# Optimization experiments

Measured on AMD Instinct MI355X. Metric: run time of the kernel, lower is better.

The kernel has to match this reference:

```python
import jax, jax.numpy as jnp
import numpy as np

B, S, E, H, C = 32, 256, 768, 512, 30
IN0 = E + 2  # LSTM layer-0 input size (770)


def _lstm_dir(x_sbf, Wih, Whh, bih, bhh, reverse):
    """One LSTM direction. x_sbf: [S,B,F]. PyTorch gate order i,f,g,o. Returns [S,B,H]."""
    h0 = jnp.zeros((x_sbf.shape[1], Whh.shape[1]), x_sbf.dtype)
    c0 = jnp.zeros_like(h0)
    xW = jnp.einsum('sbf,gf->sbg', x_sbf, Wih) + (bih + bhh)  # precompute input proj

    def step(carry, xw_t):
        h, c = carry
        gates = xw_t + h @ Whh.T
        i, f, g, o = jnp.split(gates, 4, axis=-1)
        c = jax.nn.sigmoid(f) * c + jax.nn.sigmoid(i) * jnp.tanh(g)
        h = jax.nn.sigmoid(o) * jnp.tanh(c)
        return (h, c), h

    _, ys = jax.lax.scan(step, (h0, c0), xW, reverse=reverse)
    return ys  # aligned with input time order


def _bilstm_layer(x_sbf, Wf, Uf, bif, bhf, Wb, Ub, bib, bhb):
    hf = _lstm_dir(x_sbf, Wf, Uf, bif, bhf, reverse=False)
    hb = _lstm_dir(x_sbf, Wb, Ub, bib, bhb, reverse=True)
    return jnp.concatenate([hf, hb], axis=-1)  # [S,B,2H]


def setup_inputs() -> dict:
    key = jax.random.key(0)
    ks = jax.random.split(key, 24)
    d = {
        'hidden_states': jax.random.normal(ks[0], (4, B, S, E), jnp.float32),
        'roles': jax.random.randint(ks[1], (B, S), 0, C),
        'predicates': jax.random.randint(ks[2], (B, S), 0, 2),
    }
    G = 4 * H
    shapes = {
        'Wih_l0f': (G, IN0), 'Whh_l0f': (G, H), 'bih_l0f': (G,), 'bhh_l0f': (G,),
        'Wih_l0b': (G, IN0), 'Whh_l0b': (G, H), 'bih_l0b': (G,), 'bhh_l0b': (G,),
        'Wih_l1f': (G, 2 * H), 'Whh_l1f': (G, H), 'bih_l1f': (G,), 'bhh_l1f': (G,),
        'Wih_l1b': (G, 2 * H), 'Whh_l1b': (G, H), 'bih_l1b': (G,), 'bhh_l1b': (G,),
        'W_out': (C, 2 * H), 'b_out': (C,),
    }
    for i, (name, shp) in enumerate(shapes.items()):
        d[name] = jax.random.normal(ks[3 + i], shp, jnp.float32) * 0.05
    return d


def reference(hidden_states, roles, predicates,
              Wih_l0f, Whh_l0f, bih_l0f, bhh_l0f,
              Wih_l0b, Whh_l0b, bih_l0b, bhh_l0b,
              Wih_l1f, Whh_l1f, bih_l1f, bhh_l1f,
              Wih_l1b, Whh_l1b, bih_l1b, bhh_l1b,
              W_out, b_out):
    # mean of last-4 transformer hidden states: [B,S,E]
    out = hidden_states.mean(axis=0)
    # vectorized predicate-relative features (replaces the Python .item() loops)
    idx_pred = jnp.argmax(predicates, axis=-1)                      # [B]
    mean_word = out.mean(axis=-1)                                   # [B,S]
    mean_pred = jnp.take_along_axis(mean_word, idx_pred[:, None], axis=1)  # [B,1]
    delta = mean_word - mean_pred                                   # [B,S]
    role_mask = ((roles != 0) & (roles != -100)).astype(out.dtype)  # [B,S]
    x = jnp.concatenate([out, delta[..., None], role_mask[..., None]], axis=-1)  # [B,S,E+2]

    # 2-layer BiLSTM (eval mode; inter-layer dropout inactive)
    x = jnp.swapaxes(x, 0, 1)  # [S,B,F]
    x = _bilstm_layer(x, Wih_l0f, Whh_l0f, bih_l0f, bhh_l0f,
                      Wih_l0b, Whh_l0b, bih_l0b, bhh_l0b)
    x = _bilstm_layer(x, Wih_l1f, Whh_l1f, bih_l1f, bhh_l1f,
                      Wih_l1b, Whh_l1b, bih_l1b, bhh_l1b)
    x = jnp.swapaxes(x, 0, 1)  # [B,S,2H]
    return x @ W_out.T + b_out  # [B,S,classes]
```

## Files before the change

kernel.cpp:

```cpp
#include <hip/hip_runtime.h>
#include <hip/hip_bf16.h>
#include <math.h>

#define BB 32
#define SS 256
#define EE 768
#define HH 512
#define GG 2048
#define NCLS 30
#define NWG 16

typedef __attribute__((ext_vector_type(8))) short bf16x8;
typedef __attribute__((ext_vector_type(4))) float f32x4;
typedef unsigned long long u64;

__device__ inline unsigned short f2bf(float f) {
  union { float f; unsigned int u; } v; v.f = f;
  unsigned int r = v.u + 0x7fffu + ((v.u >> 16) & 1u);
  return (unsigned short)(r >> 16);
}
__device__ inline float bf2f(unsigned short u) {
  union { unsigned int u; float f; } v; v.u = ((unsigned int)u) << 16;
  return v.f;
}
__device__ inline float sigm(float x) { return 1.f / (1.f + expf(-x)); }

__device__ inline void load_lds16(const void* g, void* l) {
  __builtin_amdgcn_global_load_lds(
      (const __attribute__((address_space(1))) void*)g,
      (__attribute__((address_space(3))) void*)l, 16, 0, 0);
}

__device__ inline u64 aload64(const u64* p) {
  return __hip_atomic_load(p, __ATOMIC_RELAXED, __HIP_MEMORY_SCOPE_AGENT);
}
__device__ inline void astore64(u64* p, u64 v) {
  __hip_atomic_store(p, v, __ATOMIC_RELAXED, __HIP_MEMORY_SCOPE_AGENT);
}

__global__ void k_convpad(const float* __restrict__ src, unsigned short* __restrict__ dst,
                          int R, int Ks, int Kd) {
  int n = R * Kd;
  for (int i = blockIdx.x * blockDim.x + threadIdx.x; i < n; i += gridDim.x * blockDim.x) {
    int r = i / Kd, k = i - r * Kd;
    dst[i] = (k < Ks) ? f2bf(src[(size_t)r * Ks + k]) : (unsigned short)0;
  }
}

__global__ void k_biassum(const float* __restrict__ a, const float* __restrict__ b,
                          float* __restrict__ o) {
  int i = blockIdx.x * 256 + threadIdx.x;
  if (i < GG) o[i] = a[i] + b[i];
}

__global__ void k_hinit(u64* __restrict__ h0, u64* __restrict__ h1) {
  int i = blockIdx.x * 256 + threadIdx.x;
  if (i < 16384) {
    u64 v = ((i >> 12) & 1) ? 0x0001000100010001ULL : 0ULL;
    h0[i] = v;
    h1[i] = v;
  }
}

__global__ void k_idxpred(const int* __restrict__ pred, int* __restrict__ idxp) {
  int b = blockIdx.x, l = threadIdx.x;
  const int* pb = pred + b * SS;
  int4 v = *(const int4*)(pb + l * 4);
  int loc = 0x7fffffff;
  if (v.w == 1) loc = 4 * l + 3;
  if (v.z == 1) loc = 4 * l + 2;
  if (v.y == 1) loc = 4 * l + 1;
  if (v.x == 1) loc = 4 * l + 0;
  for (int off = 32; off > 0; off >>= 1) {
    int o = __shfl_down(loc, off);
    loc = min(loc, o);
  }
  if (l == 0) idxp[b] = (loc == 0x7fffffff) ? 0 : loc;
}

__global__ void k_buildA0(const float* __restrict__ hs, const int* __restrict__ roles,
                          float* __restrict__ mw, unsigned short* __restrict__ A0) {
  int blk = blockIdx.x;
  int s = blk >> 5, b = blk & 31;
  unsigned short* row = A0 + (size_t)blk * 800;
  size_t base = ((size_t)b * SS + s) * EE;
  const size_t LSTR = (size_t)BB * SS * EE;
  __shared__ float red[256];
  float part = 0.f;
  for (int k = threadIdx.x; k < EE; k += 256) {
    float v = (hs[base + k] + hs[base + LSTR + k] + hs[base + 2 * LSTR + k] +
               hs[base + 3 * LSTR + k]) * 0.25f;
    part += v;
    row[k] = f2bf(v);
  }
  red[threadIdx.x] = part;
  __syncthreads();
  for (int s2 = 128; s2 > 0; s2 >>= 1) {
    if (threadIdx.x < s2) red[threadIdx.x] += red[threadIdx.x + s2];
    __syncthreads();
  }
  if (threadIdx.x == 0) mw[b * SS + s] = red[0] * (1.f / 768.f);
  if (threadIdx.x == 1) {
    int rl = roles[b * SS + s];
    row[769] = f2bf((rl != 0 && rl != -100) ? 1.f : 0.f);
  }
  if (threadIdx.x < 30) row[770 + threadIdx.x] = 0;
}

__global__ void k_predfeat(const float* __restrict__ mw, const int* __restrict__ idxp,
                           unsigned short* __restrict__ A0) {
  int i = blockIdx.x * 256 + threadIdx.x;
  int b = i >> 8, s = i & 255;
  float d = mw[i] - mw[b * SS + idxp[b]];
  A0[(size_t)(s * 32 + b) * 800 + 768] = f2bf(d);
}

__global__ __launch_bounds__(256) void k_gemm_bt(const unsigned short* __restrict__ A,
                                                 const unsigned short* __restrict__ W,
                                                 const float* __restrict__ bias,
                                                 float* __restrict__ C, int K) {
  __shared__ unsigned short As[128 * 32];
  __shared__ unsigned short Bs[128 * 32];
  const int tid = threadIdx.x;
  const int wave = tid >> 6, lane = tid & 63;
  const int l15 = lane & 15, quad = lane >> 4;
  const int m0 = blockIdx.y * 128, n0 = blockIdx.x * 128;
  const int wr = (wave >> 1) * 64, wc = (wave & 1) * 64;
  const int srow = wave * 16 + (lane >> 2);
  const int scol = (lane & 3) * 8;

  f32x4 acc[4][4];
#pragma unroll
  for (int i = 0; i < 4; i++)
#pragma unroll
    for (int j = 0; j < 4; j++) acc[i][j] = (f32x4){0.f, 0.f, 0.f, 0.f};

  for (int k0 = 0; k0 < K; k0 += 32) {
#pragma unroll
    for (int rep = 0; rep < 2; rep++) {
      load_lds16(A + (size_t)(m0 + rep * 64 + srow) * K + k0 + scol,
                 &As[(rep * 64 + wave * 16) * 32]);
      load_lds16(W + (size_t)(n0 + rep * 64 + srow) * K + k0 + scol,
                 &Bs[(rep * 64 + wave * 16) * 32]);
    }
    __syncthreads();
    bf16x8 af[4], bfr[4];
#pragma unroll
    for (int i = 0; i < 4; i++) af[i] = *(const bf16x8*)&As[(wr + i * 16 + l15) * 32 + quad * 8];
#pragma unroll
    for (int j = 0; j < 4; j++) bfr[j] = *(const bf16x8*)&Bs[(wc + j * 16 + l15) * 32 + quad * 8];
#pragma unroll
    for (int i = 0; i < 4; i++)
#pragma unroll
      for (int j = 0; j < 4; j++)
        acc[i][j] = __builtin_amdgcn_mfma_f32_16x16x32_bf16(af[i], bfr[j], acc[i][j], 0, 0, 0);
    __syncthreads();
  }

#pragma unroll
  for (int j = 0; j < 4; j++) {
    int n = n0 + wc + j * 16 + l15;
    float bv = bias[n];
#pragma unroll
    for (int i = 0; i < 4; i++) {
      int m = m0 + wr + i * 16 + quad * 4;
      int s = m >> 5, b = m & 31;
      f32x4 v = acc[i][j];
      f32x4 outv = {v[0] + bv, v[1] + bv, v[2] + bv, v[3] + bv};
      *(f32x4*)(C + ((size_t)s * GG + n) * BB + b) = outv;
    }
  }
}

__global__ __launch_bounds__(256, 1) void k_recurrent(const float* __restrict__ xWf,
                                                      const float* __restrict__ xWb,
                                                      const unsigned short* __restrict__ WhhF,
                                                      const unsigned short* __restrict__ WhhB,
                                                      u64* __restrict__ hbuf,
                                                      unsigned short* __restrict__ Hout) {
  const int wg = blockIdx.x, dir = wg >> 4, slice = wg & 15;
  const int tid = threadIdx.x, wave = tid >> 6, lane = tid & 63;
  const int l15 = lane & 15, quad = lane >> 4;
  const int u0 = slice * 32;
  const unsigned short* Whh = dir ? WhhB : WhhF;
  const float* xW = dir ? xWb : xWf;
  u64* hbT = hbuf + (size_t)dir * 8192;

  __shared__ __attribute__((aligned(16))) short hlds[32][528];
  __shared__ float gbuf[4][32][32];

  for (int i = tid; i < 32 * 264; i += 256) ((unsigned int*)hlds)[i] = 0;

  bf16x8 bfrag[2][16];
#pragma unroll
  for (int j = 0; j < 2; j++) {
    const unsigned short* wrow = Whh + (size_t)(wave * HH + u0 + j * 16 + l15) * HH + quad * 8;
#pragma unroll
    for (int kk = 0; kk < 16; kk++) bfrag[j][kk] = *(const bf16x8*)(wrow + kk * 32);
  }

  const int cb = tid >> 3;
  const int cu = (tid & 7) * 4;
  float cst[4] = {0.f, 0.f, 0.f, 0.f};

  const int guc = tid & 127;
  const int bb0 = tid >> 7;
  const bool ownCol = ((guc >> 3) == slice);

  f32x4 xv[2][2];
  {
    const int time0 = dir ? (SS - 1) : 0;
#pragma unroll
    for (int j = 0; j < 2; j++)
#pragma unroll
      for (int i = 0; i < 2; i++)
        xv[i][j] = *(const f32x4*)(xW + ((size_t)time0 * GG + wave * HH + u0 + j * 16 + l15) * BB +
                                   i * 16 + quad * 4);
  }
  __syncthreads();

  for (int t = 0; t < SS; t++) {
    const int time = dir ? (SS - 1 - t) : t;

    f32x4 acc[2][2];
#pragma unroll
    for (int i = 0; i < 2; i++)
#pragma unroll
      for (int j = 0; j < 2; j++) acc[i][j] = xv[i][j];

#pragma unroll
    for (int kk = 0; kk < 16; kk++) {
      bf16x8 a0 = *(const bf16x8*)&hlds[l15][quad * 8 + kk * 32];
      bf16x8 a1 = *(const bf16x8*)&hlds[16 + l15][quad * 8 + kk * 32];
      acc[0][0] = __builtin_amdgcn_mfma_f32_16x16x32_bf16(a0, bfrag[0][kk], acc[0][0], 0, 0, 0);
      acc[0][1] = __builtin_amdgcn_mfma_f32_16x16x32_bf16(a0, bfrag[1][kk], acc[0][1], 0, 0, 0);
      acc[1][0] = __builtin_amdgcn_mfma_f32_16x16x32_bf16(a1, bfrag[0][kk], acc[1][0], 0, 0, 0);
      acc[1][1] = __builtin_amdgcn_mfma_f32_16x16x32_bf16(a1, bfrag[1][kk], acc[1][1], 0, 0, 0);
    }
#pragma unroll
    for (int i = 0; i < 2; i++)
#pragma unroll
      for (int j = 0; j < 2; j++)
#pragma unroll
        for (int r = 0; r < 4; r++)
          gbuf[wave][i * 16 + quad * 4 + r][j * 16 + l15] = acc[i][j][r];
    __syncthreads();

    f32x4 G0 = *(const f32x4*)&gbuf[0][cb][cu];
    f32x4 G1 = *(const f32x4*)&gbuf[1][cb][cu];
    f32x4 G2 = *(const f32x4*)&gbuf[2][cb][cu];
    f32x4 G3 = *(const f32x4*)&gbuf[3][cb][cu];
    const unsigned Tb = ((unsigned)(t + 1) >> 1) & 1u;
    unsigned short hs4[4];
#pragma unroll
    for (int q = 0; q < 4; q++) {
      float gi = sigm(G0[q]), gf = sigm(G1[q]), gg = tanhf(G2[q]), go = sigm(G3[q]);
      cst[q] = gf * cst[q] + gi * gg;
      hs4[q] = (unsigned short)((f2bf(go * tanhf(cst[q])) & 0xFFFEu) | Tb);
    }
    const u64 packed =
        (u64)((unsigned)hs4[0] | ((unsigned)hs4[1] << 16)) |
        ((u64)((unsigned)hs4[2] | ((unsigned)hs4[3] << 16)) << 32);

    const int slw = (t + 1) & 1;
    astore64(hbT + slw * 4096 + (cb * 128 + ((u0 + cu) >> 2)), packed);
    *(u64*)&hlds[cb][u0 + cu] = packed;

    *(uint2*)(Hout + ((size_t)time * BB + cb) * 1024 + dir * HH + u0 + cu) =
        make_uint2((unsigned)packed, (unsigned)(packed >> 32));
    {
      const int tn = (t + 1 < SS) ? (t + 1) : t;
      const int timen = dir ? (SS - 1 - tn) : tn;
#pragma unroll
      for (int j = 0; j < 2; j++)
#pragma unroll
        for (int i = 0; i < 2; i++)
          xv[i][j] = *(const f32x4*)(xW + ((size_t)timen * GG + wave * HH + u0 + j * 16 + l15) * BB +
                                     i * 16 + quad * 4);
    }

    if (t + 1 < SS && !ownCol) {
      const u64 tmask = 0x0001000100010001ULL;
      const u64 tpat = Tb ? tmask : 0ULL;
      const u64* src = hbT + slw * 4096;
      u64 v[16];
#pragma unroll
      for (int i = 0; i < 16; i++) v[i] = aload64(src + (bb0 + 2 * i) * 128 + guc);
      for (;;) {
        unsigned st = 0;
#pragma unroll
        for (int i = 0; i < 16; i++)
          if (((v[i] ^ tpat) & tmask) != 0ULL) st |= 1u << i;
        if (!__any(st)) break;
#pragma unroll
        for (int i = 0; i < 16; i++)
          if (st & (1u << i)) v[i] = aload64(src + (bb0 + 2 * i) * 128 + guc);
      }
#pragma unroll
      for (int i = 0; i < 16; i++) *(u64*)&hlds[bb0 + 2 * i][guc * 4] = v[i];
    }
    __syncthreads();
  }
}

__global__ __launch_bounds__(256) void k_out(const unsigned short* __restrict__ H1,
                                             const float* __restrict__ Wout,
                                             const float* __restrict__ bout,
                                             float* __restrict__ out) {
  __shared__ float rows[8][1024];
  __shared__ float ps[8][32][8];
  const int rb = blockIdx.x * 8;
  const int tid = threadIdx.x;
  for (int idx = tid; idx < 8 * 1024; idx += 256) {
    int r = idx >> 10, k = idx & 1023;
    rows[r][k] = bf2f(H1[(size_t)(rb + r) * 1024 + k]);
  }
  __syncthreads();
  const int c = tid & 31, p = tid >> 5;
  float acc[8] = {0.f, 0.f, 0.f, 0.f, 0.f, 0.f, 0.f, 0.f};
  if (c < NCLS) {
    const float* wr = Wout + (size_t)c * 1024 + p * 128;
    for (int k = 0; k < 128; k++) {
      float w = wr[k];
#pragma unroll
      for (int r = 0; r < 8; r++) acc[r] += rows[r][p * 128 + k] * w;
    }
  }
#pragma unroll
  for (int r = 0; r < 8; r++) ps[p][c][r] = acc[r];
  __syncthreads();
  if (p == 0 && c < NCLS) {
    for (int r = 0; r < 8; r++) {
      float v = bout[c];
#pragma unroll
      for (int q = 0; q < 8; q++) v += ps[q][c][r];
      int row = rb + r, s = row >> 5, b = row & 31;
      out[((size_t)b * SS + s) * NCLS + c] = v;
    }
  }
}

extern "C" void kernel_launch(void* const* d_in, const int* in_sizes, int n_in,
                              void* d_out, int out_size, void* d_ws, size_t ws_size,
                              hipStream_t stream) {
  const float* hs     = (const float*)d_in[0];
  const int*   roles  = (const int*)d_in[1];
  const int*   preds  = (const int*)d_in[2];
  const float* Wih0f  = (const float*)d_in[3];
  const float* Whh0f  = (const float*)d_in[4];
  const float* bih0f  = (const float*)d_in[5];
  const float* bhh0f  = (const float*)d_in[6];
  const float* Wih0b  = (const float*)d_in[7];
  const float* Whh0b  = (const float*)d_in[8];
  const float* bih0b  = (const float*)d_in[9];
  const float* bhh0b  = (const float*)d_in[10];
  const float* Wih1f  = (const float*)d_in[11];
  const float* Whh1f  = (const float*)d_in[12];
  const float* bih1f  = (const float*)d_in[13];
  const float* bhh1f  = (const float*)d_in[14];
  const float* Wih1b  = (const float*)d_in[15];
  const float* Whh1b  = (const float*)d_in[16];
  const float* bih1b  = (const float*)d_in[17];
  const float* bhh1b  = (const float*)d_in[18];
  const float* Wout   = (const float*)d_in[19];
  const float* bout   = (const float*)d_in[20];
  (void)in_sizes; (void)n_in; (void)out_size; (void)ws_size;

  char* ws = (char*)d_ws;
  size_t off = 0;
  auto alloc = [&](size_t bytes) -> char* {
    char* p = ws + off;
    off += (bytes + 255) & ~(size_t)255;
    return p;
  };
  float* xWf = (float*)alloc((size_t)SS * GG * BB * 4);
  float* xWb = (float*)alloc((size_t)SS * GG * BB * 4);
  unsigned short* A0  = (unsigned short*)alloc((size_t)8192 * 800 * 2);
  unsigned short* H0p = (unsigned short*)alloc((size_t)8192 * 1024 * 2);
  unsigned short* H1p = (unsigned short*)alloc((size_t)8192 * 1024 * 2);
  unsigned short* Wb0f = (unsigned short*)alloc((size_t)GG * 800 * 2);
  unsigned short* Wb0b = (unsigned short*)alloc((size_t)GG * 800 * 2);
  unsigned short* Wb1f = (unsigned short*)alloc((size_t)GG * 1024 * 2);
  unsigned short* Wb1b = (unsigned short*)alloc((size_t)GG * 1024 * 2);
  unsigned short* Wh0f = (unsigned short*)alloc((size_t)GG * HH * 2);
  unsigned short* Wh0b = (unsigned short*)alloc((size_t)GG * HH * 2);
  unsigned short* Wh1f = (unsigned short*)alloc((size_t)GG * HH * 2);
  unsigned short* Wh1b = (unsigned short*)alloc((size_t)GG * HH * 2);
  float* bsum = (float*)alloc(4 * GG * 4);
  float* mw   = (float*)alloc((size_t)BB * SS * 4);
  int*   idxp = (int*)alloc(256);
  u64* hbuf0 = (u64*)alloc(131072);
  u64* hbuf1 = (u64*)alloc(131072);

  k_hinit<<<64, 256, 0, stream>>>(hbuf0, hbuf1);

  k_convpad<<<1024, 256, 0, stream>>>(Wih0f, Wb0f, GG, 770, 800);
  k_convpad<<<1024, 256, 0, stream>>>(Wih0b, Wb0b, GG, 770, 800);
  k_convpad<<<1024, 256, 0, stream>>>(Wih1f, Wb1f, GG, 1024, 1024);
  k_convpad<<<1024, 256, 0, stream>>>(Wih1b, Wb1b, GG, 1024, 1024);
  k_convpad<<<1024, 256, 0, stream>>>(Whh0f, Wh0f, GG, 512, 512);
  k_convpad<<<1024, 256, 0, stream>>>(Whh0b, Wh0b, GG, 512, 512);
  k_convpad<<<1024, 256, 0, stream>>>(Whh1f, Wh1f, GG, 512, 512);
  k_convpad<<<1024, 256, 0, stream>>>(Whh1b, Wh1b, GG, 512, 512);
  k_biassum<<<8, 256, 0, stream>>>(bih0f, bhh0f, bsum);
  k_biassum<<<8, 256, 0, stream>>>(bih0b, bhh0b, bsum + 2048);
  k_biassum<<<8, 256, 0, stream>>>(bih1f, bhh1f, bsum + 4096);
  k_biassum<<<8, 256, 0, stream>>>(bih1b, bhh1b, bsum + 6144);

  k_buildA0<<<BB * SS, 256, 0, stream>>>(hs, roles, mw, A0);
  k_idxpred<<<BB, 64, 0, stream>>>(preds, idxp);
  k_predfeat<<<32, 256, 0, stream>>>(mw, idxp, A0);

  dim3 gg(16, 64);
  k_gemm_bt<<<gg, 256, 0, stream>>>(A0, Wb0f, bsum, xWf, 800);
  k_gemm_bt<<<gg, 256, 0, stream>>>(A0, Wb0b, bsum + 2048, xWb, 800);
  k_recurrent<<<2 * NWG, 256, 0, stream>>>(xWf, xWb, Wh0f, Wh0b, hbuf0, H0p);
  k_gemm_bt<<<gg, 256, 0, stream>>>(H0p, Wb1f, bsum + 4096, xWf, 1024);
  k_gemm_bt<<<gg, 256, 0, stream>>>(H0p, Wb1b, bsum + 6144, xWb, 1024);
  k_recurrent<<<2 * NWG, 256, 0, stream>>>(xWf, xWb, Wh1f, Wh1b, hbuf1, H1p);
  k_out<<<1024, 256, 0, stream>>>(H1p, Wout, bout, (float*)d_out);
}
```

Before: 2.807 ms.

## Poll recurrent hidden-state exchange via direct global-to-LDS loads with coherent cache bits

The cross-workgroup exchange of the hidden state in the recurrent LSTM kernel now uses global_load_lds with cache-bypass flags. Each wave copies 8 full rows straight into LDS and checks the parity tag bits there, replacing per-thread 16-register atomic polling. Rows that are still stale are reloaded for up to 5 rounds, then fall back to per-element atomic spin loads. The local write of the workgroup's own slice to LDS is dropped, so every row, own slice included, is read back from global. Weight fragment loads become inline asm followed by an explicit vmcnt wait. The change aims to cut register pressure and latency in the per-timestep sync, but it depends on the coherence semantics of the cache-policy bits.

After: 2.672 ms. 4.8% less time.

```diff
diff --git a/kernel.cpp b/kernel.cpp
--- a/kernel.cpp
+++ b/kernel.cpp
@@ -30,12 +30,20 @@
       (const __attribute__((address_space(1))) void*)g,
       (__attribute__((address_space(3))) void*)l, 16, 0, 0);
 }
+__device__ inline void load_lds16c(const void* g, void* l) {
+  __builtin_amdgcn_global_load_lds(
+      (const __attribute__((address_space(1))) void*)g,
+      (__attribute__((address_space(3))) void*)l, 16, 0, 17);
+}
 
 __device__ inline u64 aload64(const u64* p) {
   return __hip_atomic_load(p, __ATOMIC_RELAXED, __HIP_MEMORY_SCOPE_AGENT);
 }
 __device__ inline void astore64(u64* p, u64 v) {
   __hip_atomic_store(p, v, __ATOMIC_RELAXED, __HIP_MEMORY_SCOPE_AGENT);
+}
+__device__ inline void wait_vm0() {
+  asm volatile("s_waitcnt vmcnt(0)" ::: "memory");
 }
 
 __global__ void k_convpad(const float* __restrict__ src, unsigned short* __restrict__ dst,
@@ -196,16 +204,16 @@
   for (int j = 0; j < 2; j++) {
     const unsigned short* wrow = Whh + (size_t)(wave * HH + u0 + j * 16 + l15) * HH + quad * 8;
 #pragma unroll
-    for (int kk = 0; kk < 16; kk++) bfrag[j][kk] = *(const bf16x8*)(wrow + kk * 32);
-  }
+    for (int kk = 0; kk < 16; kk++)
+      asm volatile("global_load_dwordx4 %0, %1, off"
+                   : "=v"(bfrag[j][kk]) : "v"(wrow + kk * 32));
+  }
+  wait_vm0();
 
   const int cb = tid >> 3;
   const int cu = (tid & 7) * 4;
   float cst[4] = {0.f, 0.f, 0.f, 0.f};
-
-  const int guc = tid & 127;
-  const int bb0 = tid >> 7;
-  const bool ownCol = ((guc >> 3) == slice);
+  const int wrow = wave * 8;
 
   f32x4 xv[2][2];
   {
@@ -264,7 +272,6 @@
 
     const int slw = (t + 1) & 1;
     astore64(hbT + slw * 4096 + (cb * 128 + ((u0 + cu) >> 2)), packed);
-    *(u64*)&hlds[cb][u0 + cu] = packed;
 
     *(uint2*)(Hout + ((size_t)time * BB + cb) * 1024 + dir * HH + u0 + cu) =
         make_uint2((unsigned)packed, (unsigned)(packed >> 32));
@@ -279,25 +286,47 @@
                                      i * 16 + quad * 4);
     }
 
-    if (t + 1 < SS && !ownCol) {
+    if (t + 1 < SS) {
       const u64 tmask = 0x0001000100010001ULL;
       const u64 tpat = Tb ? tmask : 0ULL;
-      const u64* src = hbT + slw * 4096;
-      u64 v[16];
-#pragma unroll
-      for (int i = 0; i < 16; i++) v[i] = aload64(src + (bb0 + 2 * i) * 128 + guc);
-      for (;;) {
-        unsigned st = 0;
-#pragma unroll
-        for (int i = 0; i < 16; i++)
-          if (((v[i] ^ tpat) & tmask) != 0ULL) st |= 1u << i;
-        if (!__any(st)) break;
-#pragma unroll
-        for (int i = 0; i < 16; i++)
-          if (st & (1u << i)) v[i] = aload64(src + (bb0 + 2 * i) * 128 + guc);
+      const char* srcB = (const char*)(hbT + slw * 4096);
+#pragma unroll
+      for (int r = 0; r < 8; r++)
+        load_lds16c(srcB + ((wrow + r) << 10) + (lane << 4), &hlds[wrow + r][0]);
+      unsigned stale = 0xFFFFu;
+      for (int round = 0; round < 5; round++) {
+        wait_vm0();
+        stale = 0;
+#pragma unroll
+        for (int r = 0; r < 8; r++) {
+          u64 v0 = *(const u64*)&hlds[wrow + r][8 * lane];
+          u64 v1 = *(const u64*)&hlds[wrow + r][8 * lane + 4];
+          if (((v0 ^ tpat) & tmask) != 0ULL) stale |= 1u << (2 * r);
+          if (((v1 ^ tpat) & tmask) != 0ULL) stale |= 1u << (2 * r + 1);
+        }
+        if (!__any(stale != 0)) break;
+        if (round == 4) break;
+#pragma unroll
+        for (int r = 0; r < 8; r++) {
+          if (__any((stale >> (2 * r)) & 3))
+            load_lds16c(srcB + ((wrow + r) << 10) + (lane << 4), &hlds[wrow + r][0]);
+        }
       }
-#pragma unroll
-      for (int i = 0; i < 16; i++) *(u64*)&hlds[bb0 + 2 * i][guc * 4] = v[i];
+      if (__any(stale != 0)) {
+        const u64* src = hbT + slw * 4096;
+#pragma unroll
+        for (int r = 0; r < 8; r++) {
+#pragma unroll
+          for (int c = 0; c < 2; c++) {
+            if ((stale >> (2 * r + c)) & 1) {
+              const int g = (wrow + r) * 128 + 2 * lane + c;
+              u64 x = aload64(src + g);
+              while (((x ^ tpat) & tmask) != 0ULL) x = aload64(src + g);
+              *(u64*)&hlds[wrow + r][8 * lane + 4 * c] = x;
+            }
+          }
+        }
+      }
     }
     __syncthreads();
   }
```
